# Kernel optimization log

Hardware: AMD Instinct MI355X
Metric: run time of the kernel (lower is better)

Reference implementation:

```python
import jax, jax.numpy as jnp
import numpy as np

B, D, K, H = 8192, 1024, 4096, 8


def setup_inputs() -> dict:
    key = jax.random.key(0)
    k1, k2 = jax.random.split(key)
    inputs = jax.random.normal(k1, (B, 1, D), dtype=jnp.float32)
    # Per-head codebooks; original init decays scale by init_decay_weight**hix,
    # emulate with a 0.5**h decay so later heads model smaller residuals.
    decay = (0.5 ** jnp.arange(H, dtype=jnp.float32)).reshape(H, 1, 1)
    codebooks = jax.random.normal(k2, (H, K, D), dtype=jnp.float32) * decay
    return {"inputs": inputs, "codebooks": codebooks}


def reference(inputs, codebooks):
    """Hierarchical refinement quantizer, eval path (hard argmin selection).

    Cascade over heads: distances to codebook -> argmin -> gather embedding
    -> subtract from residual -> next head. Returns (quantized_sum, codes).
    """
    x = inputs[:, 0, :]                      # [B, D]
    resid = x
    quantized = jnp.zeros_like(x)
    codes = []
    n_heads = codebooks.shape[0]
    for h in range(n_heads):                 # fixed, small head count
        E = codebooks[h]                     # [K, D]
        # squared euclidean distances: ||r||^2 - 2 r.E^T + ||E||^2  -> [B, K]
        dist = (
            jnp.sum(resid * resid, axis=-1, keepdims=True)
            - 2.0 * jnp.einsum("bd,kd->bk", resid, E)
            + jnp.sum(E * E, axis=-1)
        )
        idx = jnp.argmin(dist, axis=-1)      # [B]
        onehot = jax.nn.one_hot(idx, E.shape[0], dtype=resid.dtype)  # [B, K]
        q = onehot @ E                       # [B, D] gathered embedding
        quantized = quantized + q
        resid = resid - q
        codes.append(idx)
    vq_codes = jnp.stack(codes, axis=1)      # [B, H]
    return quantized, vq_codes
```

## Files before the change

### kernel.cpp

```cpp
#include <hip/hip_runtime.h>

#define B_ 8192
#define D_ 1024
#define K_ 4096
#define H_ 8

#define BM 128
#define BN 128
#define BK 32
#define NBLK 64
#define NCAND 6

typedef __attribute__((ext_vector_type(8))) short short8v;
typedef __attribute__((ext_vector_type(4))) float f32x4;

#define FINF 3.4e38f
#define IBIG 0x7fffffff

__device__ __forceinline__ void amin(float& v, int& i, float v2, int i2) {
    if (v2 < v || (v2 == v && i2 < i)) { v = v2; i = i2; }
}

__device__ __forceinline__ unsigned short f2bf_rn(float x) {
    unsigned int u = __float_as_uint(x);
    unsigned int r = (u + 0x7fffu + ((u >> 16) & 1u)) >> 16;
    return (unsigned short)r;
}

__device__ __forceinline__ void gload16(const unsigned short* g, unsigned short* l) {
    __builtin_amdgcn_global_load_lds(
        (const __attribute__((address_space(1))) void*)g,
        (__attribute__((address_space(3))) void*)l, 16, 0, 0);
}

__global__ __launch_bounds__(256) void cbconv_kernel(const float* __restrict__ E,
                                                     unsigned short* __restrict__ hi,
                                                     float* __restrict__ eeh) {
    const int row = blockIdx.x;
    const int t = threadIdx.x;
    float4 v = reinterpret_cast<const float4*>(E + (size_t)row * D_)[t];
    ushort4 h;
    h.x = f2bf_rn(v.x); h.y = f2bf_rn(v.y);
    h.z = f2bf_rn(v.z); h.w = f2bf_rn(v.w);
    reinterpret_cast<ushort4*>(hi + (size_t)row * D_)[t] = h;
    float s = v.x * v.x + v.y * v.y + v.z * v.z + v.w * v.w;
    #pragma unroll
    for (int m = 1; m < 64; m <<= 1) s += __shfl_xor(s, m);
    __shared__ float ls[4];
    if ((t & 63) == 0) ls[t >> 6] = s;
    __syncthreads();
    if (t == 0) eeh[row] = (ls[0] + ls[1]) + (ls[2] + ls[3]);
}

__global__ __launch_bounds__(256) void init_kernel(const float* __restrict__ x,
                                                   float* __restrict__ resid,
                                                   float* __restrict__ rr,
                                                   unsigned short* __restrict__ rhi) {
    const int b = blockIdx.x;
    const int t = threadIdx.x;
    float4 v = reinterpret_cast<const float4*>(x + (size_t)b * D_)[t];
    reinterpret_cast<float4*>(resid + (size_t)b * D_)[t] = v;
    ushort4 h;
    h.x = f2bf_rn(v.x); h.y = f2bf_rn(v.y);
    h.z = f2bf_rn(v.z); h.w = f2bf_rn(v.w);
    reinterpret_cast<ushort4*>(rhi + (size_t)b * D_)[t] = h;
    float s = v.x * v.x + v.y * v.y + v.z * v.z + v.w * v.w;
    #pragma unroll
    for (int m = 1; m < 64; m <<= 1) s += __shfl_xor(s, m);
    __shared__ float ls[4];
    if ((t & 63) == 0) ls[t >> 6] = s;
    __syncthreads();
    if (t == 0) rr[b] = (ls[0] + ls[1]) + (ls[2] + ls[3]);
}

__global__ __launch_bounds__(256) void score_mfma_kernel(
    const unsigned short* __restrict__ Ch,
    const unsigned short* __restrict__ Rh,
    const float* __restrict__ ee,
    float* __restrict__ pval, int* __restrict__ pidx) {
    __shared__ unsigned short lds[2][128][BK];

    const int tid = threadIdx.x;
    const int bid = blockIdx.x;
    const int xcd = bid & 7;
    const int r_  = bid >> 3;
    const int bx  = (xcd << 2) | (r_ & 3);
    const int by  = r_ >> 2;
    const int be0 = bx * BN;
    const int br0 = by * BM;

    f32x4 acc[4][4];
    #pragma unroll
    for (int i = 0; i < 4; ++i)
        #pragma unroll
        for (int j = 0; j < 4; ++j)
            #pragma unroll
            for (int r = 0; r < 4; ++r) acc[i][j][r] = 0.f;

    const int srow = tid >> 2;
    const int sch  = (tid & 3) * 8;
    const size_t rstep = (size_t)64 * D_;
    const unsigned short* pC = Ch + (size_t)(be0 + srow) * D_ + sch;
    const unsigned short* pR = Rh + (size_t)(br0 + srow) * D_ + sch;

    const int l  = tid & 63;
    const int w  = tid >> 6;
    const int wr = (w >> 1) * 64;
    const int wc = (w & 1) * 64;
    const int fr = l & 15;
    const int k8 = (l >> 4) * 8;

    for (int d0 = 0; d0 < D_; d0 += BK) {
        __syncthreads();
        gload16(pC + d0,         &lds[0][srow][sch]);
        gload16(pC + rstep + d0, &lds[0][srow + 64][sch]);
        gload16(pR + d0,         &lds[1][srow][sch]);
        gload16(pR + rstep + d0, &lds[1][srow + 64][sch]);
        __syncthreads();

        short8v a_h[4], b_h[4];
        #pragma unroll
        for (int f = 0; f < 4; ++f) {
            a_h[f] = *reinterpret_cast<const short8v*>(&lds[0][wr + f * 16 + fr][k8]);
            b_h[f] = *reinterpret_cast<const short8v*>(&lds[1][wc + f * 16 + fr][k8]);
        }
        #pragma unroll
        for (int i = 0; i < 4; ++i)
            #pragma unroll
            for (int j = 0; j < 4; ++j)
                acc[i][j] = __builtin_amdgcn_mfma_f32_16x16x32_bf16(a_h[i], b_h[j], acc[i][j], 0, 0, 0);
    }

    const int g4 = (l >> 4) * 4;
    float eb[4][4];
    int ec[4][4];
    #pragma unroll
    for (int i = 0; i < 4; ++i)
        #pragma unroll
        for (int r = 0; r < 4; ++r) {
            ec[i][r] = be0 + wr + i * 16 + g4 + r;
            eb[i][r] = ee[ec[i][r]];
        }
    const int eblk = bx * 2 + (w >> 1);

    #pragma unroll
    for (int j = 0; j < 4; ++j) {
        const int rrow = br0 + wc + j * 16 + fr;
        float b1 = FINF; int i1 = IBIG;
        float b2 = FINF; int i2 = IBIG;
        #pragma unroll
        for (int i = 0; i < 4; ++i)
            #pragma unroll
            for (int r = 0; r < 4; ++r) {
                const float s = fmaf(-2.0f, acc[i][j][r], eb[i][r]);
                const int c = ec[i][r];
                const bool lt = (s < b1) || (s == b1 && c < i1);
                const float lv = lt ? b1 : s;
                const int   li = lt ? i1 : c;
                if (lt) { b1 = s; i1 = c; }
                amin(b2, i2, lv, li);
            }
        #pragma unroll
        for (int m = 16; m < 64; m <<= 1) {
            const float o1 = __shfl_xor(b1, m); const int oi1 = __shfl_xor(i1, m);
            const float o2 = __shfl_xor(b2, m); const int oi2 = __shfl_xor(i2, m);
            const bool lt = (o1 < b1) || (o1 == b1 && oi1 < i1);
            const float lv = lt ? b1 : o1;
            const int   li = lt ? i1 : oi1;
            if (lt) { b1 = o1; i1 = oi1; }
            amin(b2, i2, o2, oi2);
            amin(b2, i2, lv, li);
        }
        if ((l >> 4) == 0) {
            const size_t base = ((size_t)rrow * NBLK + eblk) * 2;
            pval[base] = b1;     pidx[base] = i1;
            pval[base + 1] = b2; pidx[base + 1] = i2;
        }
    }
}

__global__ __launch_bounds__(256) void update_kernel(
    float* __restrict__ resid,
    const float* __restrict__ E,
    const float* __restrict__ ee,
    const float* __restrict__ pval,
    const int* __restrict__ pidx,
    float* __restrict__ rr,
    float* __restrict__ codes,
    unsigned short* __restrict__ rhi,
    const float* __restrict__ x,
    float* __restrict__ quant,
    int h) {
    const int w = threadIdx.x >> 6;
    const int l = threadIdx.x & 63;
    const int b = blockIdx.x * 4 + w;

    const size_t pbase = ((size_t)b * NBLK + l) * 2;
    float v0 = pval[pbase], v1 = pval[pbase + 1];
    int i0 = pidx[pbase], i1 = pidx[pbase + 1];
    int cand[NCAND];
    #pragma unroll
    for (int r = 0; r < NCAND; ++r) {
        float av = v0; int ai = i0;
        amin(av, ai, v1, i1);
        #pragma unroll
        for (int m = 1; m < 64; m <<= 1) {
            float ov = __shfl_xor(av, m);
            int oi = __shfl_xor(ai, m);
            amin(av, ai, ov, oi);
        }
        if (ai == i0) v0 = FINF;
        if (ai == i1) v1 = FINF;
        cand[r] = ai;
    }

    const float4* r4row = reinterpret_cast<const float4*>(resid + (size_t)b * D_);
    float4 rx[4];
    #pragma unroll
    for (int q = 0; q < 4; ++q) rx[q] = r4row[q * 64 + l];

    float dots[NCAND];
    #pragma unroll
    for (int c = 0; c < NCAND; ++c) {
        const float4* e4 = reinterpret_cast<const float4*>(E + (size_t)cand[c] * D_);
        float dot = 0.f;
        #pragma unroll
        for (int q = 0; q < 4; ++q) {
            float4 e = e4[q * 64 + l];
            dot = fmaf(rx[q].x, e.x, dot);
            dot = fmaf(rx[q].y, e.y, dot);
            dot = fmaf(rx[q].z, e.z, dot);
            dot = fmaf(rx[q].w, e.w, dot);
        }
        #pragma unroll
        for (int m = 1; m < 64; m <<= 1) dot += __shfl_xor(dot, m);
        dots[c] = dot;
    }

    const float rv = rr[b];
    float bv = FINF; int bi = IBIG;
    #pragma unroll
    for (int c = 0; c < NCAND; ++c) {
        const float s = (rv - 2.0f * dots[c]) + ee[cand[c]];
        amin(bv, bi, s, cand[c]);
    }
    if (l == 0) codes[(size_t)b * H_ + h] = (float)bi;

    const float4* q4 = reinterpret_cast<const float4*>(E + (size_t)bi * D_);
    float4* r4w = reinterpret_cast<float4*>(resid + (size_t)b * D_);
    ushort4* h4w = reinterpret_cast<ushort4*>(rhi + (size_t)b * D_);
    float nrm = 0.f;
    #pragma unroll
    for (int q = 0; q < 4; ++q) {
        float4 qv = q4[q * 64 + l];
        float4 r = rx[q];
        r.x -= qv.x; r.y -= qv.y; r.z -= qv.z; r.w -= qv.w;
        rx[q] = r;
        r4w[q * 64 + l] = r;
        ushort4 hh;
        hh.x = f2bf_rn(r.x); hh.y = f2bf_rn(r.y);
        hh.z = f2bf_rn(r.z); hh.w = f2bf_rn(r.w);
        h4w[q * 64 + l] = hh;
        nrm += r.x * r.x + r.y * r.y + r.z * r.z + r.w * r.w;
    }
    #pragma unroll
    for (int m = 1; m < 64; m <<= 1) nrm += __shfl_xor(nrm, m);
    if (l == 0) rr[b] = nrm;

    if (h == H_ - 1) {
        const float4* x4 = reinterpret_cast<const float4*>(x + (size_t)b * D_);
        float4* o4 = reinterpret_cast<float4*>(quant + (size_t)b * D_);
        #pragma unroll
        for (int q = 0; q < 4; ++q) {
            float4 xv = x4[q * 64 + l];
            float4 o;
            o.x = xv.x - rx[q].x; o.y = xv.y - rx[q].y;
            o.z = xv.z - rx[q].z; o.w = xv.w - rx[q].w;
            o4[q * 64 + l] = o;
        }
    }
}

extern "C" void kernel_launch(void* const* d_in, const int* in_sizes, int n_in,
                              void* d_out, int out_size, void* d_ws, size_t ws_size,
                              hipStream_t stream) {
    const float* x  = (const float*)d_in[0];
    const float* cb = (const float*)d_in[1];
    float* out = (float*)d_out;
    float* quant = out;
    float* codes = out + (size_t)B_ * D_;

    char* ws = (char*)d_ws;
    size_t off = 0;
    float* resid = (float*)(ws + off); off += (size_t)B_ * D_ * 4;
    float* rr    = (float*)(ws + off); off += (size_t)B_ * 4;
    float* ee    = (float*)(ws + off); off += (size_t)H_ * K_ * 4;
    float* pval  = (float*)(ws + off); off += (size_t)B_ * NBLK * 2 * 4;
    int*   pidx  = (int*)  (ws + off); off += (size_t)B_ * NBLK * 2 * 4;
    unsigned short* rhi = (unsigned short*)(ws + off); off += (size_t)B_ * D_ * 2;
    unsigned short* chi = (unsigned short*)(ws + off); off += (size_t)K_ * D_ * 2;

    hipLaunchKernelGGL(init_kernel, dim3(B_), dim3(256), 0, stream, x, resid, rr, rhi);

    for (int h = 0; h < H_; ++h) {
        const float* E  = cb + (size_t)h * K_ * D_;
        float* eh = ee + (size_t)h * K_;
        hipLaunchKernelGGL(cbconv_kernel, dim3(K_), dim3(256), 0, stream, E, chi, eh);
        hipLaunchKernelGGL(score_mfma_kernel, dim3((K_ / BN) * (B_ / BM)), dim3(256),
                           0, stream, chi, rhi, eh, pval, pidx);
        hipLaunchKernelGGL(update_kernel, dim3(B_ / 4), dim3(256), 0, stream,
                           resid, E, eh, pval, pidx, rr, codes, rhi, x, quant, h);
    }
}
```

Measured before the change: 1.156 ms.

## Enlarge score tile to 256x128 and keep top-3 candidates per block

```diff
diff --git a/kernel.cpp b/kernel.cpp
--- a/kernel.cpp
+++ b/kernel.cpp
@@ -5,11 +5,12 @@
 #define K_ 4096
 #define H_ 8
 
-#define BM 128
-#define BN 128
+#define BE 256
+#define BR 128
 #define BK 32
-#define NBLK 64
-#define NCAND 6
+#define NBLK 32
+#define TOPB 3
+#define NCAND 8
 
 typedef __attribute__((ext_vector_type(8))) short short8v;
 typedef __attribute__((ext_vector_type(4))) float f32x4;
@@ -73,25 +74,26 @@
     if (t == 0) rr[b] = (ls[0] + ls[1]) + (ls[2] + ls[3]);
 }
 
-__global__ __launch_bounds__(256) void score_mfma_kernel(
+__global__ __launch_bounds__(256, 2) void score_mfma_kernel(
     const unsigned short* __restrict__ Ch,
     const unsigned short* __restrict__ Rh,
     const float* __restrict__ ee,
     float* __restrict__ pval, int* __restrict__ pidx) {
-    __shared__ unsigned short lds[2][128][BK];
+    __shared__ unsigned short ldsE[BE][BK];
+    __shared__ unsigned short ldsR[BR][BK];
 
     const int tid = threadIdx.x;
     const int bid = blockIdx.x;
     const int xcd = bid & 7;
     const int r_  = bid >> 3;
-    const int bx  = (xcd << 2) | (r_ & 3);
-    const int by  = r_ >> 2;
-    const int be0 = bx * BN;
-    const int br0 = by * BM;
-
-    f32x4 acc[4][4];
-    #pragma unroll
-    for (int i = 0; i < 4; ++i)
+    const int bx  = (xcd << 1) | (r_ & 1);
+    const int by  = r_ >> 1;
+    const int be0 = bx * BE;
+    const int br0 = by * BR;
+
+    f32x4 acc[8][4];
+    #pragma unroll
+    for (int i = 0; i < 8; ++i)
         #pragma unroll
         for (int j = 0; j < 4; ++j)
             #pragma unroll
@@ -100,83 +102,90 @@
     const int srow = tid >> 2;
     const int sch  = (tid & 3) * 8;
     const size_t rstep = (size_t)64 * D_;
-    const unsigned short* pC = Ch + (size_t)(be0 + srow) * D_ + sch;
+    const unsigned short* pE = Ch + (size_t)(be0 + srow) * D_ + sch;
     const unsigned short* pR = Rh + (size_t)(br0 + srow) * D_ + sch;
 
     const int l  = tid & 63;
     const int w  = tid >> 6;
-    const int wr = (w >> 1) * 64;
-    const int wc = (w & 1) * 64;
+    const int wE = w >> 1;
+    const int wR = w & 1;
     const int fr = l & 15;
     const int k8 = (l >> 4) * 8;
 
     for (int d0 = 0; d0 < D_; d0 += BK) {
         __syncthreads();
-        gload16(pC + d0,         &lds[0][srow][sch]);
-        gload16(pC + rstep + d0, &lds[0][srow + 64][sch]);
-        gload16(pR + d0,         &lds[1][srow][sch]);
-        gload16(pR + rstep + d0, &lds[1][srow + 64][sch]);
+        #pragma unroll
+        for (int c = 0; c < 4; ++c)
+            gload16(pE + c * rstep + d0, &ldsE[srow + c * 64][sch]);
+        #pragma unroll
+        for (int c = 0; c < 2; ++c)
+            gload16(pR + c * rstep + d0, &ldsR[srow + c * 64][sch]);
         __syncthreads();
 
-        short8v a_h[4], b_h[4];
-        #pragma unroll
-        for (int f = 0; f < 4; ++f) {
-            a_h[f] = *reinterpret_cast<const short8v*>(&lds[0][wr + f * 16 + fr][k8]);
-            b_h[f] = *reinterpret_cast<const short8v*>(&lds[1][wc + f * 16 + fr][k8]);
-        }
-        #pragma unroll
-        for (int i = 0; i < 4; ++i)
+        short8v af[8], bf[4];
+        #pragma unroll
+        for (int i = 0; i < 8; ++i)
+            af[i] = *reinterpret_cast<const short8v*>(&ldsE[wE * 128 + i * 16 + fr][k8]);
+        #pragma unroll
+        for (int j = 0; j < 4; ++j)
+            bf[j] = *reinterpret_cast<const short8v*>(&ldsR[wR * 64 + j * 16 + fr][k8]);
+        #pragma unroll
+        for (int i = 0; i < 8; ++i)
             #pragma unroll
             for (int j = 0; j < 4; ++j)
-                acc[i][j] = __builtin_amdgcn_mfma_f32_16x16x32_bf16(a_h[i], b_h[j], acc[i][j], 0, 0, 0);
+                acc[i][j] = __builtin_amdgcn_mfma_f32_16x16x32_bf16(af[i], bf[j], acc[i][j], 0, 0, 0);
     }
 
     const int g4 = (l >> 4) * 4;
-    float eb[4][4];
-    int ec[4][4];
-    #pragma unroll
-    for (int i = 0; i < 4; ++i)
+    float ev[8][4];
+    int ecd[8][4];
+    #pragma unroll
+    for (int i = 0; i < 8; ++i)
         #pragma unroll
         for (int r = 0; r < 4; ++r) {
-            ec[i][r] = be0 + wr + i * 16 + g4 + r;
-            eb[i][r] = ee[ec[i][r]];
-        }
-    const int eblk = bx * 2 + (w >> 1);
+            ecd[i][r] = be0 + wE * 128 + i * 16 + g4 + r;
+            ev[i][r] = ee[ecd[i][r]];
+        }
+    const int eblk = bx * 2 + wE;
+
+    #define INS3(v, c) do {                                         \
+        const float _v = (v); const int _c = (c);                   \
+        if (_v < b1 || (_v == b1 && _c < i1)) {                     \
+            b3 = b2; i3 = i2; b2 = b1; i2 = i1; b1 = _v; i1 = _c;   \
+        } else if (_v < b2 || (_v == b2 && _c < i2)) {              \
+            b3 = b2; i3 = i2; b2 = _v; i2 = _c;                     \
+        } else if (_v < b3 || (_v == b3 && _c < i3)) {              \
+            b3 = _v; i3 = _c;                                       \
+        }                                                           \
+    } while (0)
 
     #pragma unroll
     for (int j = 0; j < 4; ++j) {
-        const int rrow = br0 + wc + j * 16 + fr;
-        float b1 = FINF; int i1 = IBIG;
-        float b2 = FINF; int i2 = IBIG;
-        #pragma unroll
-        for (int i = 0; i < 4; ++i)
+        const int rrow = br0 + wR * 64 + j * 16 + fr;
+        float b1 = FINF, b2 = FINF, b3 = FINF;
+        int i1 = IBIG, i2 = IBIG, i3 = IBIG;
+        #pragma unroll
+        for (int i = 0; i < 8; ++i)
             #pragma unroll
             for (int r = 0; r < 4; ++r) {
-                const float s = fmaf(-2.0f, acc[i][j][r], eb[i][r]);
-                const int c = ec[i][r];
-                const bool lt = (s < b1) || (s == b1 && c < i1);
-                const float lv = lt ? b1 : s;
-                const int   li = lt ? i1 : c;
-                if (lt) { b1 = s; i1 = c; }
-                amin(b2, i2, lv, li);
+                const float s = fmaf(-2.0f, acc[i][j][r], ev[i][r]);
+                INS3(s, ecd[i][r]);
             }
         #pragma unroll
         for (int m = 16; m < 64; m <<= 1) {
             const float o1 = __shfl_xor(b1, m); const int oi1 = __shfl_xor(i1, m);
             const float o2 = __shfl_xor(b2, m); const int oi2 = __shfl_xor(i2, m);
-            const bool lt = (o1 < b1) || (o1 == b1 && oi1 < i1);
-            const float lv = lt ? b1 : o1;
-            const int   li = lt ? i1 : oi1;
-            if (lt) { b1 = o1; i1 = oi1; }
-            amin(b2, i2, o2, oi2);
-            amin(b2, i2, lv, li);
+            const float o3 = __shfl_xor(b3, m); const int oi3 = __shfl_xor(i3, m);
+            INS3(o1, oi1); INS3(o2, oi2); INS3(o3, oi3);
         }
         if ((l >> 4) == 0) {
-            const size_t base = ((size_t)rrow * NBLK + eblk) * 2;
+            const size_t base = ((size_t)rrow * NBLK + eblk) * TOPB;
             pval[base] = b1;     pidx[base] = i1;
             pval[base + 1] = b2; pidx[base + 1] = i2;
-        }
-    }
+            pval[base + 2] = b3; pidx[base + 2] = i3;
+        }
+    }
+    #undef INS3
 }
 
 __global__ __launch_bounds__(256) void update_kernel(
@@ -195,14 +204,20 @@
     const int l = threadIdx.x & 63;
     const int b = blockIdx.x * 4 + w;
 
-    const size_t pbase = ((size_t)b * NBLK + l) * 2;
-    float v0 = pval[pbase], v1 = pval[pbase + 1];
-    int i0 = pidx[pbase], i1 = pidx[pbase + 1];
+    float v0 = FINF, v1 = FINF, v2 = FINF;
+    int i0 = IBIG, i1 = IBIG, i2 = IBIG;
+    if (l < NBLK) {
+        const size_t pbase = ((size_t)b * NBLK + l) * TOPB;
+        v0 = pval[pbase];     i0 = pidx[pbase];
+        v1 = pval[pbase + 1]; i1 = pidx[pbase + 1];
+        v2 = pval[pbase + 2]; i2 = pidx[pbase + 2];
+    }
     int cand[NCAND];
     #pragma unroll
     for (int r = 0; r < NCAND; ++r) {
         float av = v0; int ai = i0;
         amin(av, ai, v1, i1);
+        amin(av, ai, v2, i2);
         #pragma unroll
         for (int m = 1; m < 64; m <<= 1) {
             float ov = __shfl_xor(av, m);
@@ -211,6 +226,7 @@
         }
         if (ai == i0) v0 = FINF;
         if (ai == i1) v1 = FINF;
+        if (ai == i2) v2 = FINF;
         cand[r] = ai;
     }
 
@@ -295,8 +311,8 @@
     float* resid = (float*)(ws + off); off += (size_t)B_ * D_ * 4;
     float* rr    = (float*)(ws + off); off += (size_t)B_ * 4;
     float* ee    = (float*)(ws + off); off += (size_t)H_ * K_ * 4;
-    float* pval  = (float*)(ws + off); off += (size_t)B_ * NBLK * 2 * 4;
-    int*   pidx  = (int*)  (ws + off); off += (size_t)B_ * NBLK * 2 * 4;
+    float* pval  = (float*)(ws + off); off += (size_t)B_ * NBLK * TOPB * 4;
+    int*   pidx  = (int*)  (ws + off); off += (size_t)B_ * NBLK * TOPB * 4;
     unsigned short* rhi = (unsigned short*)(ws + off); off += (size_t)B_ * D_ * 2;
     unsigned short* chi = (unsigned short*)(ws + off); off += (size_t)K_ * D_ * 2;
 
@@ -306,7 +322,7 @@
         const float* E  = cb + (size_t)h * K_ * D_;
         float* eh = ee + (size_t)h * K_;
         hipLaunchKernelGGL(cbconv_kernel, dim3(K_), dim3(256), 0, stream, E, chi, eh);
-        hipLaunchKernelGGL(score_mfma_kernel, dim3((K_ / BN) * (B_ / BM)), dim3(256),
+        hipLaunchKernelGGL(score_mfma_kernel, dim3((K_ / BE) * (B_ / BR)), dim3(256),
                            0, stream, chi, rhi, eh, pval, pidx);
         hipLaunchKernelGGL(update_kernel, dim3(B_ / 4), dim3(256), 0, stream,
                            resid, E, eh, pval, pidx, rr, codes, rhi, x, quant, h);
```

Result: slower. 1.306 ms (+12.9%).
